# Kernel tuning notes

Hardware: AMD Instinct MI355X
Metric: run time of the kernel (lower is better)

## Reference

```python
import jax, jax.numpy as jnp
import numpy as np

N_EMBED = 1024
HEAD_SIZE = 128

def setup_inputs() -> dict:
    key = jax.random.key(0)
    k1, k2, k3, k4 = jax.random.split(key, 4)
    x = jax.random.normal(k1, (8, 2048, N_EMBED), dtype=jnp.float32)
    # torch.nn.Linear default init: U(-1/sqrt(in), 1/sqrt(in)); stored as [out, in],
    # we store transposed [in, out] for x @ W.
    bound = 1.0 / np.sqrt(N_EMBED)
    Wk = jax.random.uniform(k2, (N_EMBED, HEAD_SIZE), jnp.float32, -bound, bound)
    Wq = jax.random.uniform(k3, (N_EMBED, HEAD_SIZE), jnp.float32, -bound, bound)
    Wv = jax.random.uniform(k4, (N_EMBED, HEAD_SIZE), jnp.float32, -bound, bound)
    return {"x": x, "Wk": Wk, "Wq": Wq, "Wv": Wv}

def reference(x, Wk, Wq, Wv):
    # x: [B, T, E]
    k = jnp.einsum('bte,eh->bth', x, Wk)  # [B, T, H]
    q = jnp.einsum('bte,eh->bth', x, Wq)
    v = jnp.einsum('bte,eh->bth', x, Wv)
    scale = 1.0 / np.sqrt(HEAD_SIZE).astype(np.float32)
    wei = jnp.einsum('bqh,bkh->bqk', q, k) * scale  # [B, T, T]
    wei = jax.nn.softmax(wei, axis=-1)
    out = jnp.einsum('bqk,bkh->bqh', wei, v)  # [B, T, H]
    return out
```

## Files before the change

kernel.cpp:

```cpp
#include <hip/hip_runtime.h>

#define BATCH 8
#define TLEN 2048
#define EMB 1024
#define HDIM 128
#define SCALE 0.08838834764831845f
#define NSPLIT 4

typedef _Float16 f16x8 __attribute__((ext_vector_type(8)));
typedef _Float16 f16x4 __attribute__((ext_vector_type(4)));
typedef float f32x4 __attribute__((ext_vector_type(4)));

static __device__ __forceinline__ f32x4 mfma16(f16x8 a, f16x8 b, f32x4 c) {
    return __builtin_amdgcn_mfma_f32_16x16x32_f16(a, b, c, 0, 0, 0);
}

__global__ void prep_w(const float* __restrict__ Wk, const float* __restrict__ Wq,
                       const float* __restrict__ Wv, _Float16* __restrict__ wtf) {
    int g = blockIdx.x * 256 + threadIdx.x;
    int lane = g & 63;
    int kstep = (g >> 6) & 31;
    int ntile = g >> 11;
    int n = ntile * 16 + (lane & 15);
    int sel = n >> 7;
    int h = n & 127;
    const float* W = (sel == 0) ? Wk : (sel == 1) ? Wq : Wv;
    int kbase = kstep * 32 + (lane >> 4) * 8;
    f16x8 o;
#pragma unroll
    for (int j = 0; j < 8; j++) {
        float v = W[(size_t)(kbase + j) * HDIM + h];
        if (sel == 1) v *= SCALE;
        o[j] = (_Float16)v;
    }
    *(f16x8*)&wtf[(size_t)g * 8] = o;
}

__global__ __launch_bounds__(256, 2) void proj_kernel(
        const float* __restrict__ x, const _Float16* __restrict__ wtf,
        _Float16* __restrict__ kb, _Float16* __restrict__ qb, _Float16* __restrict__ vbT) {
    __shared__ _Float16 xs[32 * 72];
    const int t = threadIdx.x;
    const int m0 = blockIdx.x * 32;
    const int wv = t >> 6;
    const int lane = t & 63;
    const int m16 = lane & 15;
    const int quad = lane >> 4;
    const int n0 = wv * 96;

    const f32x4 zero4 = {0.f, 0.f, 0.f, 0.f};
    f32x4 acc[2][6];
#pragma unroll
    for (int mt = 0; mt < 2; mt++)
#pragma unroll
        for (int nt = 0; nt < 6; nt++) acc[mt][nt] = zero4;

    for (int k0 = 0; k0 < EMB; k0 += 64) {
        f16x8 bf[2][6];
#pragma unroll
        for (int ks = 0; ks < 2; ks++) {
            int kstep = (k0 >> 5) + ks;
#pragma unroll
            for (int nt = 0; nt < 6; nt++) {
                int ntile = wv * 6 + nt;
                bf[ks][nt] = *(const f16x8*)
                    &wtf[(size_t)((ntile * 32 + kstep) * 64 + lane) * 8];
            }
        }
        float4 xv[2];
#pragma unroll
        for (int i = 0; i < 2; i++) {
            int u = t + i * 256;
            xv[i] = *(const float4*)&x[(size_t)(m0 + (u >> 4)) * EMB + k0 + (u & 15) * 4];
        }
        __syncthreads();
#pragma unroll
        for (int i = 0; i < 2; i++) {
            int u = t + i * 256;
            f16x4 h;
            h[0] = (_Float16)xv[i].x; h[1] = (_Float16)xv[i].y;
            h[2] = (_Float16)xv[i].z; h[3] = (_Float16)xv[i].w;
            *(f16x4*)&xs[(u >> 4) * 72 + (u & 15) * 4] = h;
        }
        __syncthreads();
#pragma unroll
        for (int ks = 0; ks < 2; ks++) {
            f16x8 af[2];
#pragma unroll
            for (int mt = 0; mt < 2; mt++)
                af[mt] = *(const f16x8*)&xs[(mt * 16 + m16) * 72 + ks * 32 + quad * 8];
#pragma unroll
            for (int mt = 0; mt < 2; mt++)
#pragma unroll
                for (int nt = 0; nt < 6; nt++)
                    acc[mt][nt] = mfma16(af[mt], bf[ks][nt], acc[mt][nt]);
        }
    }
#pragma unroll
    for (int nt = 0; nt < 6; nt++) {
        int n = n0 + nt * 16 + m16;
        int nsel = n >> 7;
        int h = n & 127;
        if (nsel < 2) {
            _Float16* dst = (nsel == 0) ? kb : qb;
#pragma unroll
            for (int mt = 0; mt < 2; mt++)
#pragma unroll
                for (int r = 0; r < 4; r++) {
                    int mg = m0 + mt * 16 + quad * 4 + r;
                    dst[(size_t)mg * HDIM + h] = (_Float16)acc[mt][nt][r];
                }
        } else {
#pragma unroll
            for (int mt = 0; mt < 2; mt++) {
                int mg = m0 + mt * 16 + quad * 4;
                int bb = mg >> 11, tok = mg & 2047;
                f16x4 pk;
#pragma unroll
                for (int r = 0; r < 4; r++) pk[r] = (_Float16)acc[mt][nt][r];
                *(f16x4*)&vbT[((size_t)bb * HDIM + h) * TLEN + tok] = pk;
            }
        }
    }
}

__global__ __launch_bounds__(256, 2) void attn_kernel(
        const _Float16* __restrict__ qb, const _Float16* __restrict__ kb,
        const _Float16* __restrict__ vbT,
        float* __restrict__ po, float* __restrict__ pl) {
    __shared__ _Float16 kls[64 * 136];
    __shared__ _Float16 vtl[128 * 72];
    __shared__ _Float16 pls[4 * 32 * 72];
    const int t = threadIdx.x;
    const int qt = blockIdx.x;
    const int b = blockIdx.y;
    const int sp = blockIdx.z;
    const int wv = t >> 6;
    const int lane = t & 63;
    const int m16 = lane & 15;
    const int quad = lane >> 4;
    const int q0 = qt * 128 + wv * 32;
    _Float16* pw = pls + wv * (32 * 72);

    f16x8 qf[2][4];
#pragma unroll
    for (int mt = 0; mt < 2; mt++)
#pragma unroll
        for (int ks = 0; ks < 4; ks++)
            qf[mt][ks] = *(const f16x8*)
                &qb[((size_t)b * TLEN + q0 + mt * 16 + m16) * HDIM + ks * 32 + quad * 8];

    f16x8 ones;
#pragma unroll
    for (int j = 0; j < 8; j++) ones[j] = (_Float16)1.0f;

    const f32x4 zero4 = {0.f, 0.f, 0.f, 0.f};
    f32x4 o[2][8], ol[2];
#pragma unroll
    for (int mt = 0; mt < 2; mt++) {
        ol[mt] = zero4;
#pragma unroll
        for (int nt = 0; nt < 8; nt++) o[mt][nt] = zero4;
    }

    for (int kt = sp * 8; kt < sp * 8 + 8; kt++) {
        const int k0 = kt * 64;
        f16x8 kreg[4], vreg[4];
#pragma unroll
        for (int rep = 0; rep < 4; rep++) {
            int u = t + rep * 256;
            kreg[rep] = *(const f16x8*)
                &kb[((size_t)b * TLEN + k0 + (u >> 4)) * HDIM + (u & 15) * 8];
            vreg[rep] = *(const f16x8*)
                &vbT[((size_t)b * HDIM + (u >> 3)) * TLEN + k0 + (u & 7) * 8];
        }
        __syncthreads();
#pragma unroll
        for (int rep = 0; rep < 4; rep++) {
            int u = t + rep * 256;
            *(f16x8*)&kls[(u >> 4) * 136 + (u & 15) * 8] = kreg[rep];
            *(f16x8*)&vtl[(u >> 3) * 72 + (u & 7) * 8] = vreg[rep];
        }
        __syncthreads();
        f32x4 st[4][2];
#pragma unroll
        for (int kt_ = 0; kt_ < 4; kt_++) {
            st[kt_][0] = zero4; st[kt_][1] = zero4;
#pragma unroll
            for (int ks = 0; ks < 4; ks++) {
                f16x8 kf = *(const f16x8*)&kls[(kt_ * 16 + m16) * 136 + ks * 32 + quad * 8];
                st[kt_][0] = mfma16(kf, qf[0][ks], st[kt_][0]);
                st[kt_][1] = mfma16(kf, qf[1][ks], st[kt_][1]);
            }
        }
#pragma unroll
        for (int kt_ = 0; kt_ < 4; kt_++)
#pragma unroll
            for (int mt = 0; mt < 2; mt++) {
                f16x4 pk;
#pragma unroll
                for (int r = 0; r < 4; r++)
                    pk[r] = (_Float16)__expf(st[kt_][mt][r]);
                *(f16x4*)&pw[(mt * 16 + m16) * 72 + kt_ * 16 + quad * 4] = pk;
            }
        f16x8 ap[2][2];
#pragma unroll
        for (int mt = 0; mt < 2; mt++)
#pragma unroll
            for (int kc = 0; kc < 2; kc++)
                ap[mt][kc] = *(const f16x8*)&pw[(mt * 16 + m16) * 72 + kc * 32 + quad * 8];
#pragma unroll
        for (int mt = 0; mt < 2; mt++) {
            ol[mt] = mfma16(ap[mt][0], ones, ol[mt]);
            ol[mt] = mfma16(ap[mt][1], ones, ol[mt]);
        }
#pragma unroll
        for (int nt = 0; nt < 8; nt++) {
            f16x8 b0 = *(const f16x8*)&vtl[(nt * 16 + m16) * 72 + quad * 8];
            f16x8 b1 = *(const f16x8*)&vtl[(nt * 16 + m16) * 72 + 32 + quad * 8];
            o[0][nt] = mfma16(ap[0][0], b0, o[0][nt]);
            o[0][nt] = mfma16(ap[0][1], b1, o[0][nt]);
            o[1][nt] = mfma16(ap[1][0], b0, o[1][nt]);
            o[1][nt] = mfma16(ap[1][1], b1, o[1][nt]);
        }
    }
#pragma unroll
    for (int mt = 0; mt < 2; mt++)
#pragma unroll
        for (int r = 0; r < 4; r++) {
            int row = q0 + mt * 16 + quad * 4 + r;
            size_t prow = ((size_t)(sp * BATCH + b)) * TLEN + row;
#pragma unroll
            for (int nt = 0; nt < 8; nt++)
                po[prow * HDIM + nt * 16 + m16] = o[mt][nt][r];
            if (m16 == 0) pl[prow] = ol[mt][r];
        }
}

__global__ void combine_kernel(const float* __restrict__ po, const float* __restrict__ pl,
                               float* __restrict__ out) {
    int g = blockIdx.x * 256 + threadIdx.x;
    int row = g >> 5;
    int part = g & 31;
    int bb = row >> 11;
    int tok = row & 2047;
    float L = 0.f;
    float4 acc = {0.f, 0.f, 0.f, 0.f};
#pragma unroll
    for (int s = 0; s < NSPLIT; s++) {
        size_t prow = ((size_t)(s * BATCH + bb)) * TLEN + tok;
        L += pl[prow];
        float4 p = *(const float4*)&po[prow * HDIM + part * 4];
        acc.x += p.x; acc.y += p.y; acc.z += p.z; acc.w += p.w;
    }
    float inv = 1.f / L;
    float4 res = {acc.x * inv, acc.y * inv, acc.z * inv, acc.w * inv};
    *(float4*)&out[(size_t)row * HDIM + part * 4] = res;
}

extern "C" void kernel_launch(void* const* d_in, const int* in_sizes, int n_in,
                              void* d_out, int out_size, void* d_ws, size_t ws_size,
                              hipStream_t stream) {
    const float* x  = (const float*)d_in[0];
    const float* Wk = (const float*)d_in[1];
    const float* Wq = (const float*)d_in[2];
    const float* Wv = (const float*)d_in[3];
    float* out = (float*)d_out;
    char* ws = (char*)d_ws;
    _Float16* wtf = (_Float16*)(ws);
    _Float16* kb  = (_Float16*)(ws + (1ull << 20));
    _Float16* qb  = (_Float16*)(ws + (5ull << 20));
    _Float16* vbT = (_Float16*)(ws + (9ull << 20));
    float* po = (float*)(ws + (13ull << 20));
    float* pl = (float*)(ws + (13ull << 20) + 33554432ull);

    prep_w<<<dim3(192), dim3(256), 0, stream>>>(Wk, Wq, Wv, wtf);
    proj_kernel<<<dim3(512), dim3(256), 0, stream>>>(x, wtf, kb, qb, vbT);
    attn_kernel<<<dim3(16, BATCH, NSPLIT), dim3(256), 0, stream>>>(qb, kb, vbT, po, pl);
    combine_kernel<<<dim3(2048), dim3(256), 0, stream>>>(po, pl, out);
}
```

Measured before the change: 157.9 us.

## Double-buffer projection loads, fp16 partial outputs, scalar row sums in attention

The projection kernel now double-buffers x and weight fragments in registers and shared memory, so the next tile's global loads are issued before the current tile's MFMAs and one barrier per step is removed. In the attention kernel, row sums are accumulated in scalars with a final shuffle reduction instead of extra MFMAs against a ones vector. Partial outputs are stored as fp16 to halve the traffic written by attention and read by the combine step. LDS padding is changed, and the occupancy hint goes from 2 to 3 blocks per CU. Storing unnormalized partial sums in fp16 loses precision, and the pl pointer is moved to a new offset.

```diff
diff --git a/kernel.cpp b/kernel.cpp
--- a/kernel.cpp
+++ b/kernel.cpp
@@ -39,7 +39,7 @@
 __global__ __launch_bounds__(256, 2) void proj_kernel(
         const float* __restrict__ x, const _Float16* __restrict__ wtf,
         _Float16* __restrict__ kb, _Float16* __restrict__ qb, _Float16* __restrict__ vbT) {
-    __shared__ _Float16 xs[32 * 72];
+    __shared__ _Float16 xs[2][32 * 72];
     const int t = threadIdx.x;
     const int m0 = blockIdx.x * 32;
     const int wv = t >> 6;
@@ -47,6 +47,8 @@
     const int m16 = lane & 15;
     const int quad = lane >> 4;
     const int n0 = wv * 96;
+    const int r0 = t >> 4;
+    const int c0 = (t & 15) * 4;
 
     const f32x4 zero4 = {0.f, 0.f, 0.f, 0.f};
     f32x4 acc[2][6];
@@ -55,45 +57,50 @@
 #pragma unroll
         for (int nt = 0; nt < 6; nt++) acc[mt][nt] = zero4;
 
-    for (int k0 = 0; k0 < EMB; k0 += 64) {
-        f16x8 bf[2][6];
+    const float* xrow0 = &x[(size_t)(m0 + r0) * EMB + c0];
+    const float* xrow1 = &x[(size_t)(m0 + 16 + r0) * EMB + c0];
+
+    float4 xv[2][2];
+    f16x8 bf[2][12];
+    xv[0][0] = *(const float4*)(xrow0);
+    xv[0][1] = *(const float4*)(xrow1);
+#pragma unroll
+    for (int ks = 0; ks < 2; ks++)
+#pragma unroll
+        for (int nt = 0; nt < 6; nt++)
+            bf[0][ks * 6 + nt] = *(const f16x8*)
+                &wtf[((size_t)((wv * 6 + nt) * 32 + ks) * 64 + lane) * 8];
+
+#pragma unroll
+    for (int it = 0; it < 16; it++) {
+        const int cur = it & 1, nxt = cur ^ 1;
+#pragma unroll
+        for (int i = 0; i < 2; i++) {
+            f16x4 h;
+            h[0] = (_Float16)xv[cur][i].x; h[1] = (_Float16)xv[cur][i].y;
+            h[2] = (_Float16)xv[cur][i].z; h[3] = (_Float16)xv[cur][i].w;
+            *(f16x4*)&xs[cur][(r0 + 16 * i) * 72 + c0] = h;
+        }
+        __syncthreads();
+        if (it < 15) {
+            xv[nxt][0] = *(const float4*)(xrow0 + (it + 1) * 64);
+            xv[nxt][1] = *(const float4*)(xrow1 + (it + 1) * 64);
+#pragma unroll
+            for (int ks = 0; ks < 2; ks++)
+#pragma unroll
+                for (int nt = 0; nt < 6; nt++)
+                    bf[nxt][ks * 6 + nt] = *(const f16x8*)
+                        &wtf[((size_t)((wv * 6 + nt) * 32 + (it + 1) * 2 + ks) * 64 + lane) * 8];
+        }
 #pragma unroll
         for (int ks = 0; ks < 2; ks++) {
-            int kstep = (k0 >> 5) + ks;
+            f16x8 a0 = *(const f16x8*)&xs[cur][m16 * 72 + ks * 32 + quad * 8];
+            f16x8 a1 = *(const f16x8*)&xs[cur][(16 + m16) * 72 + ks * 32 + quad * 8];
 #pragma unroll
             for (int nt = 0; nt < 6; nt++) {
-                int ntile = wv * 6 + nt;
-                bf[ks][nt] = *(const f16x8*)
-                    &wtf[(size_t)((ntile * 32 + kstep) * 64 + lane) * 8];
-            }
-        }
-        float4 xv[2];
-#pragma unroll
-        for (int i = 0; i < 2; i++) {
-            int u = t + i * 256;
-            xv[i] = *(const float4*)&x[(size_t)(m0 + (u >> 4)) * EMB + k0 + (u & 15) * 4];
-        }
-        __syncthreads();
-#pragma unroll
-        for (int i = 0; i < 2; i++) {
-            int u = t + i * 256;
-            f16x4 h;
-            h[0] = (_Float16)xv[i].x; h[1] = (_Float16)xv[i].y;
-            h[2] = (_Float16)xv[i].z; h[3] = (_Float16)xv[i].w;
-            *(f16x4*)&xs[(u >> 4) * 72 + (u & 15) * 4] = h;
-        }
-        __syncthreads();
-#pragma unroll
-        for (int ks = 0; ks < 2; ks++) {
-            f16x8 af[2];
-#pragma unroll
-            for (int mt = 0; mt < 2; mt++)
-                af[mt] = *(const f16x8*)&xs[(mt * 16 + m16) * 72 + ks * 32 + quad * 8];
-#pragma unroll
-            for (int mt = 0; mt < 2; mt++)
-#pragma unroll
-                for (int nt = 0; nt < 6; nt++)
-                    acc[mt][nt] = mfma16(af[mt], bf[ks][nt], acc[mt][nt]);
+                acc[0][nt] = mfma16(a0, bf[cur][ks * 6 + nt], acc[0][nt]);
+                acc[1][nt] = mfma16(a1, bf[cur][ks * 6 + nt], acc[1][nt]);
+            }
         }
     }
 #pragma unroll
@@ -124,12 +131,12 @@
     }
 }
 
-__global__ __launch_bounds__(256, 2) void attn_kernel(
+__global__ __launch_bounds__(256, 3) void attn_kernel(
         const _Float16* __restrict__ qb, const _Float16* __restrict__ kb,
         const _Float16* __restrict__ vbT,
-        float* __restrict__ po, float* __restrict__ pl) {
-    __shared__ _Float16 kls[64 * 136];
-    __shared__ _Float16 vtl[128 * 72];
+        _Float16* __restrict__ po, float* __restrict__ pl) {
+    __shared__ _Float16 kls[64 * 132];
+    __shared__ _Float16 vtl[128 * 68];
     __shared__ _Float16 pls[4 * 32 * 72];
     const int t = threadIdx.x;
     const int qt = blockIdx.x;
@@ -150,59 +157,59 @@
             qf[mt][ks] = *(const f16x8*)
                 &qb[((size_t)b * TLEN + q0 + mt * 16 + m16) * HDIM + ks * 32 + quad * 8];
 
-    f16x8 ones;
-#pragma unroll
-    for (int j = 0; j < 8; j++) ones[j] = (_Float16)1.0f;
-
     const f32x4 zero4 = {0.f, 0.f, 0.f, 0.f};
-    f32x4 o[2][8], ol[2];
-#pragma unroll
-    for (int mt = 0; mt < 2; mt++) {
-        ol[mt] = zero4;
+    f32x4 o[2][8];
+    float lacc[2] = {0.f, 0.f};
+#pragma unroll
+    for (int mt = 0; mt < 2; mt++)
 #pragma unroll
         for (int nt = 0; nt < 8; nt++) o[mt][nt] = zero4;
-    }
 
     for (int kt = sp * 8; kt < sp * 8 + 8; kt++) {
         const int k0 = kt * 64;
-        f16x8 kreg[4], vreg[4];
+        f16x8 kreg[4];
 #pragma unroll
         for (int rep = 0; rep < 4; rep++) {
             int u = t + rep * 256;
             kreg[rep] = *(const f16x8*)
                 &kb[((size_t)b * TLEN + k0 + (u >> 4)) * HDIM + (u & 15) * 8];
-            vreg[rep] = *(const f16x8*)
-                &vbT[((size_t)b * HDIM + (u >> 3)) * TLEN + k0 + (u & 7) * 8];
         }
         __syncthreads();
 #pragma unroll
         for (int rep = 0; rep < 4; rep++) {
             int u = t + rep * 256;
-            *(f16x8*)&kls[(u >> 4) * 136 + (u & 15) * 8] = kreg[rep];
-            *(f16x8*)&vtl[(u >> 3) * 72 + (u & 7) * 8] = vreg[rep];
+            *(f16x8*)&kls[(u >> 4) * 132 + (u & 15) * 8] = kreg[rep];
+        }
+#pragma unroll
+        for (int rep = 0; rep < 4; rep++) {
+            int u = t + rep * 256;
+            f16x8 v = *(const f16x8*)
+                &vbT[((size_t)b * HDIM + (u >> 3)) * TLEN + k0 + (u & 7) * 8];
+            *(f16x8*)&vtl[(u >> 3) * 68 + (u & 7) * 8] = v;
         }
         __syncthreads();
-        f32x4 st[4][2];
 #pragma unroll
         for (int kt_ = 0; kt_ < 4; kt_++) {
-            st[kt_][0] = zero4; st[kt_][1] = zero4;
+            f32x4 st0 = zero4, st1 = zero4;
 #pragma unroll
             for (int ks = 0; ks < 4; ks++) {
-                f16x8 kf = *(const f16x8*)&kls[(kt_ * 16 + m16) * 136 + ks * 32 + quad * 8];
-                st[kt_][0] = mfma16(kf, qf[0][ks], st[kt_][0]);
-                st[kt_][1] = mfma16(kf, qf[1][ks], st[kt_][1]);
-            }
-        }
-#pragma unroll
-        for (int kt_ = 0; kt_ < 4; kt_++)
-#pragma unroll
-            for (int mt = 0; mt < 2; mt++) {
-                f16x4 pk;
-#pragma unroll
-                for (int r = 0; r < 4; r++)
-                    pk[r] = (_Float16)__expf(st[kt_][mt][r]);
-                *(f16x4*)&pw[(mt * 16 + m16) * 72 + kt_ * 16 + quad * 4] = pk;
-            }
+                f16x8 kf = *(const f16x8*)&kls[(kt_ * 16 + m16) * 132 + ks * 32 + quad * 8];
+                st0 = mfma16(kf, qf[0][ks], st0);
+                st1 = mfma16(kf, qf[1][ks], st1);
+            }
+            f16x4 p0, p1;
+#pragma unroll
+            for (int r = 0; r < 4; r++) {
+                float e0 = __expf(st0[r]);
+                float e1 = __expf(st1[r]);
+                lacc[0] += e0;
+                lacc[1] += e1;
+                p0[r] = (_Float16)e0;
+                p1[r] = (_Float16)e1;
+            }
+            *(f16x4*)&pw[m16 * 72 + kt_ * 16 + quad * 4] = p0;
+            *(f16x4*)&pw[(16 + m16) * 72 + kt_ * 16 + quad * 4] = p1;
+        }
         f16x8 ap[2][2];
 #pragma unroll
         for (int mt = 0; mt < 2; mt++)
@@ -210,14 +217,9 @@
             for (int kc = 0; kc < 2; kc++)
                 ap[mt][kc] = *(const f16x8*)&pw[(mt * 16 + m16) * 72 + kc * 32 + quad * 8];
 #pragma unroll
-        for (int mt = 0; mt < 2; mt++) {
-            ol[mt] = mfma16(ap[mt][0], ones, ol[mt]);
-            ol[mt] = mfma16(ap[mt][1], ones, ol[mt]);
-        }
-#pragma unroll
         for (int nt = 0; nt < 8; nt++) {
-            f16x8 b0 = *(const f16x8*)&vtl[(nt * 16 + m16) * 72 + quad * 8];
-            f16x8 b1 = *(const f16x8*)&vtl[(nt * 16 + m16) * 72 + 32 + quad * 8];
+            f16x8 b0 = *(const f16x8*)&vtl[(nt * 16 + m16) * 68 + quad * 8];
+            f16x8 b1 = *(const f16x8*)&vtl[(nt * 16 + m16) * 68 + 32 + quad * 8];
             o[0][nt] = mfma16(ap[0][0], b0, o[0][nt]);
             o[0][nt] = mfma16(ap[0][1], b1, o[0][nt]);
             o[1][nt] = mfma16(ap[1][0], b0, o[1][nt]);
@@ -225,19 +227,26 @@
         }
     }
 #pragma unroll
-    for (int mt = 0; mt < 2; mt++)
+    for (int mt = 0; mt < 2; mt++) {
+        lacc[mt] += __shfl_xor(lacc[mt], 16);
+        lacc[mt] += __shfl_xor(lacc[mt], 32);
+    }
+#pragma unroll
+    for (int mt = 0; mt < 2; mt++) {
+        if (quad == 0)
+            pl[((size_t)(sp * BATCH + b)) * TLEN + q0 + mt * 16 + m16] = lacc[mt];
 #pragma unroll
         for (int r = 0; r < 4; r++) {
             int row = q0 + mt * 16 + quad * 4 + r;
             size_t prow = ((size_t)(sp * BATCH + b)) * TLEN + row;
 #pragma unroll
             for (int nt = 0; nt < 8; nt++)
-                po[prow * HDIM + nt * 16 + m16] = o[mt][nt][r];
-            if (m16 == 0) pl[prow] = ol[mt][r];
-        }
-}
-
-__global__ void combine_kernel(const float* __restrict__ po, const float* __restrict__ pl,
+                po[prow * HDIM + nt * 16 + m16] = (_Float16)o[mt][nt][r];
+        }
+    }
+}
+
+__global__ void combine_kernel(const _Float16* __restrict__ po, const float* __restrict__ pl,
                                float* __restrict__ out) {
     int g = blockIdx.x * 256 + threadIdx.x;
     int row = g >> 5;
@@ -250,8 +259,9 @@
     for (int s = 0; s < NSPLIT; s++) {
         size_t prow = ((size_t)(s * BATCH + bb)) * TLEN + tok;
         L += pl[prow];
-        float4 p = *(const float4*)&po[prow * HDIM + part * 4];
-        acc.x += p.x; acc.y += p.y; acc.z += p.z; acc.w += p.w;
+        f16x4 p = *(const f16x4*)&po[prow * HDIM + part * 4];
+        acc.x += (float)p[0]; acc.y += (float)p[1];
+        acc.z += (float)p[2]; acc.w += (float)p[3];
     }
     float inv = 1.f / L;
     float4 res = {acc.x * inv, acc.y * inv, acc.z * inv, acc.w * inv};
@@ -271,8 +281,8 @@
     _Float16* kb  = (_Float16*)(ws + (1ull << 20));
     _Float16* qb  = (_Float16*)(ws + (5ull << 20));
     _Float16* vbT = (_Float16*)(ws + (9ull << 20));
-    float* po = (float*)(ws + (13ull << 20));
-    float* pl = (float*)(ws + (13ull << 20) + 33554432ull);
+    _Float16* po  = (_Float16*)(ws + (13ull << 20));
+    float* pl = (float*)(ws + (29ull << 20));
 
     prep_w<<<dim3(192), dim3(256), 0, stream>>>(Wk, Wq, Wv, wtf);
     proj_kernel<<<dim3(512), dim3(256), 0, stream>>>(x, wtf, kb, qb, vbT);
```

Result: no change. 157.7 us (-0.1%).
